# Optimization experiments

Hardware: AMD Instinct MI355X
Metric: run time of the kernel (lower is better)

## Reference

```python
import jax, jax.numpy as jnp
import numpy as np

B, S, E, H = 2, 2048, 1024, 16
DH = E // H  # 64


def setup_inputs() -> dict:
    key = jax.random.key(0)
    ks = jax.random.split(key, 13)
    s = 1.0 / np.sqrt(E)
    inp = {
        'query': jax.random.normal(ks[0], (B, S, E), jnp.float32),
        'key':   jax.random.normal(ks[1], (B, S, E), jnp.float32),
        'value': jax.random.normal(ks[2], (B, S, E), jnp.float32),
        # nn.Linear weights stored [out, in]
        'Wq': jax.random.uniform(ks[3], (E, E), jnp.float32, -s, s),
        'bq': jax.random.uniform(ks[4], (E,), jnp.float32, -s, s),
        'Wk': jax.random.uniform(ks[5], (E, E), jnp.float32, -s, s),
        'bk': jax.random.uniform(ks[6], (E,), jnp.float32, -s, s),
        'Wv': jax.random.uniform(ks[7], (E, E), jnp.float32, -s, s),
        'bv': jax.random.uniform(ks[8], (E,), jnp.float32, -s, s),
        # 1x1 Conv2d over head channels: weight [H, H] (squeezed from [H,H,1,1]), bias [H]
        'Wc': jax.random.uniform(ks[9], (H, H), jnp.float32, -1.0 / np.sqrt(H), 1.0 / np.sqrt(H)),
        'bc': jax.random.uniform(ks[10], (H,), jnp.float32, -1.0 / np.sqrt(H), 1.0 / np.sqrt(H)),
        'Wo': jax.random.uniform(ks[11], (E, E), jnp.float32, -s, s),
        'bo': jax.random.uniform(ks[12], (E,), jnp.float32, -s, s),
    }
    return inp


def reference(query, key, value, Wq, bq, Wk, bk, Wv, bv, Wc, bc, Wo, bo):
    b, s = query.shape[0], query.shape[1]
    # projections -> (B, H, S, Dh)
    def split_heads(x):
        return x.reshape(b, s, H, DH).transpose(0, 2, 1, 3)
    Q = split_heads(query @ Wq.T + bq)
    K = split_heads(key @ Wk.T + bk)
    V = split_heads(value @ Wv.T + bv)
    # raw scores (B, H, S, S)
    scores = jnp.einsum('bhqd,bhkd->bhqk', Q, K) / np.sqrt(DH).astype(np.float32)
    # 1x1 conv mixes logits across heads: channel-wise matmul + bias
    noise = jnp.einsum('gh,bhqk->bgqk', Wc, scores) + bc[None, :, None, None]
    scores = scores + noise
    weights = jax.nn.softmax(scores, axis=-1)
    out = jnp.einsum('bhqk,bhkd->bhqd', weights, V)  # (B, H, S, Dh)
    out = out.transpose(0, 2, 1, 3).reshape(b, s, E)
    return out @ Wo.T + bo
```

## Files before the change

### kernel.cpp

```cpp
#include <hip/hip_runtime.h>


typedef __attribute__((ext_vector_type(8))) short bf16x8_t;
typedef __attribute__((ext_vector_type(4))) float f32x4_t;

__device__ inline unsigned short f2bf(float f) {
  unsigned u = __builtin_bit_cast(unsigned, f);
  u += 0x7fffu + ((u >> 16) & 1u);
  return (unsigned short)(u >> 16);
}

struct ConvArgs {
  const float* src[7];
  unsigned short* dst[7];
  int n[7];
};

__global__ __launch_bounds__(256) void convert_f32_bf16(ConvArgs a) {
  const int which = blockIdx.y;
  const int i = (blockIdx.x * 256 + threadIdx.x) * 8;
  if (i >= a.n[which]) return;
  const float* s = a.src[which] + i;
  f32x4_t x0 = *(const f32x4_t*)(s);
  f32x4_t x1 = *(const f32x4_t*)(s + 4);
  bf16x8_t o;
#pragma unroll
  for (int j = 0; j < 4; j++) o[j] = (short)f2bf(x0[j]);
#pragma unroll
  for (int j = 0; j < 4; j++) o[4 + j] = (short)f2bf(x1[j]);
  *(bf16x8_t*)(a.dst[which] + i) = o;
}

__global__ __launch_bounds__(256) void gemm_bt(
    const unsigned short* __restrict__ A, const unsigned short* __restrict__ Bt,
    const float* __restrict__ bias, void* __restrict__ C,
    int M, int N, int K, int c_is_f32)
{
  __shared__ unsigned short As[128 * 32];
  __shared__ unsigned short Bs[128 * 32];
  const int t = threadIdx.x;
  const int l = t & 63;
  const int w = t >> 6;
  const int quad = l >> 4, n16 = l & 15;
  const int wm = (w & 1) * 64, wn = (w >> 1) * 64;
  const long m0 = (long)blockIdx.x * 128, n0 = (long)blockIdx.y * 128;

  f32x4_t acc[4][4] = {};

  const unsigned short* gA = A + (m0 + (t >> 2)) * (long)K + (t & 3) * 8;
  const unsigned short* gB = Bt + (n0 + (t >> 2)) * (long)K + (t & 3) * 8;
  const long rowskip = 64l * K;

  for (int kt = 0; kt < K; kt += 32) {
    bf16x8_t ra0 = *(const bf16x8_t*)(gA + kt);
    bf16x8_t ra1 = *(const bf16x8_t*)(gA + kt + rowskip);
    bf16x8_t rb0 = *(const bf16x8_t*)(gB + kt);
    bf16x8_t rb1 = *(const bf16x8_t*)(gB + kt + rowskip);
    __syncthreads();
    *(bf16x8_t*)&As[t * 8] = ra0;
    *(bf16x8_t*)&As[2048 + t * 8] = ra1;
    *(bf16x8_t*)&Bs[t * 8] = rb0;
    *(bf16x8_t*)&Bs[2048 + t * 8] = rb1;
    __syncthreads();
    bf16x8_t af[4], bfr[4];
#pragma unroll
    for (int i = 0; i < 4; i++) {
      af[i]  = *(const bf16x8_t*)&As[(wm + i * 16 + n16) * 32 + quad * 8];
      bfr[i] = *(const bf16x8_t*)&Bs[(wn + i * 16 + n16) * 32 + quad * 8];
    }
#pragma unroll
    for (int mi = 0; mi < 4; mi++)
#pragma unroll
      for (int ni = 0; ni < 4; ni++)
        acc[mi][ni] = __builtin_amdgcn_mfma_f32_16x16x32_bf16(af[mi], bfr[ni], acc[mi][ni], 0, 0, 0);
  }

#pragma unroll
  for (int ni = 0; ni < 4; ni++) {
    const long n = n0 + wn + ni * 16 + n16;
    const float bv = bias[n];
#pragma unroll
    for (int mi = 0; mi < 4; mi++) {
#pragma unroll
      for (int r = 0; r < 4; r++) {
        const long m = m0 + wm + mi * 16 + quad * 4 + r;
        const float v = acc[mi][ni][r] + bv;
        if (c_is_f32) ((float*)C)[m * N + n] = v;
        else ((unsigned short*)C)[m * N + n] = f2bf(v);
      }
    }
  }
}

__global__ __launch_bounds__(256) void transpose_v(
    const unsigned short* __restrict__ V, unsigned short* __restrict__ VT)
{
  __shared__ unsigned short tile[64][72];
  const int t = threadIdx.x;
  const int s0 = blockIdx.x * 64, h = blockIdx.y, b = blockIdx.z;
#pragma unroll
  for (int r = 0; r < 2; r++) {
    const int elem = r * 2048 + t * 8;
    const int s = elem >> 6, d = elem & 63;
    *(bf16x8_t*)&tile[s][d] =
        *(const bf16x8_t*)&V[(size_t)(b * 2048 + s0 + s) * 1024 + h * 64 + d];
  }
  __syncthreads();
#pragma unroll
  for (int r = 0; r < 2; r++) {
    const int elem = r * 2048 + t * 8;
    const int d = elem >> 6, sl = elem & 63;
    bf16x8_t o;
#pragma unroll
    for (int j = 0; j < 8; j++) o[j] = (short)tile[sl + j][d];
    *(bf16x8_t*)&VT[((size_t)(b * 16 + h) * 64 + d) * 2048 + s0 + sl] = o;
  }
}

__global__ __launch_bounds__(1024) void attention_fused(
    const unsigned short* __restrict__ Qb, const unsigned short* __restrict__ Kb,
    const unsigned short* __restrict__ VT, const float* __restrict__ Wc,
    unsigned short* __restrict__ Obuf)
{
  __shared__ unsigned short sraw[512 * 40];
  __shared__ float sprime[16 * 580];
  __shared__ unsigned short pbuf[16][16 * 40];
  __shared__ unsigned short mmat[16 * 32];

  const int t = threadIdx.x;
  const int g = t >> 6, l = t & 63;
  const int quad = l >> 4, n16 = l & 15;
  const int qb = blockIdx.x, b = blockIdx.y;
  const int q0 = qb * 16;

  for (int i = t; i < 512 * 40; i += 1024) sraw[i] = 0;
  if (t < 256) {
    const int gg = t >> 4, hh = t & 15;
    const float v = (((gg == hh) ? 1.0f : 0.0f) + Wc[gg * 16 + hh]) * 0.125f;
    mmat[gg * 32 + hh] = f2bf(v);
  } else if (t < 512) {
    const int t2 = t - 256;
    mmat[(t2 >> 4) * 32 + 16 + (t2 & 15)] = 0;
  }
  __syncthreads();

  const bf16x8_t mfrag = *(const bf16x8_t*)&mmat[n16 * 32 + quad * 8];
  bf16x8_t qf[2];
#pragma unroll
  for (int dr = 0; dr < 2; dr++)
    qf[dr] = *(const bf16x8_t*)&Qb[(size_t)(b * 2048 + q0 + n16) * 1024 + g * 64 + dr * 32 + quad * 8];

  f32x4_t o[4] = {};
  float m_run = -1e30f, l_run = 0.0f;
  const int qrow = l >> 2, kpos = (l & 3) * 8;

  for (int kt = 0; kt < 2048; kt += 32) {
    bf16x8_t kf[2][2], vf[4];
#pragma unroll
    for (int kc = 0; kc < 2; kc++)
#pragma unroll
      for (int dr = 0; dr < 2; dr++)
        kf[kc][dr] = *(const bf16x8_t*)&Kb[(size_t)(b * 2048 + kt + kc * 16 + n16) * 1024
                                           + g * 64 + dr * 32 + quad * 8];
#pragma unroll
    for (int dc = 0; dc < 4; dc++)
      vf[dc] = *(const bf16x8_t*)&VT[((size_t)(b * 16 + g) * 64 + dc * 16 + n16) * 2048
                                      + kt + quad * 8];

    f32x4_t sfrag[2] = {};
#pragma unroll
    for (int kc = 0; kc < 2; kc++)
#pragma unroll
      for (int dr = 0; dr < 2; dr++)
        sfrag[kc] = __builtin_amdgcn_mfma_f32_16x16x32_bf16(qf[dr], kf[kc][dr], sfrag[kc], 0, 0, 0);

#pragma unroll
    for (int kc = 0; kc < 2; kc++)
#pragma unroll
      for (int r = 0; r < 4; r++) {
        const int col = (quad * 4 + r) * 32 + kc * 16 + n16;
        sraw[col * 40 + g] = f2bf(sfrag[kc][r]);
      }
    __syncthreads();

    f32x4_t mixd[2];
#pragma unroll
    for (int c2 = 0; c2 < 2; c2++) {
      const int c = g * 2 + c2;
      const bf16x8_t bb = *(const bf16x8_t*)&sraw[(c * 16 + n16) * 40 + quad * 8];
      f32x4_t z = {};
      mixd[c2] = __builtin_amdgcn_mfma_f32_16x16x32_bf16(mfrag, bb, z, 0, 0, 0);
    }
#pragma unroll
    for (int c2 = 0; c2 < 2; c2++) {
      const int c = g * 2 + c2;
      const int qq = c >> 1;
      const int kk = (c & 1) * 16 + n16;
#pragma unroll
      for (int r = 0; r < 4; r++)
        sprime[(quad * 4 + r) * 580 + qq * 36 + kk] = mixd[c2][r];
    }
    __syncthreads();

    const float* rowp = &sprime[g * 580 + qrow * 36 + kpos];
    const f32x4_t x0 = *(const f32x4_t*)rowp;
    const f32x4_t x1 = *(const f32x4_t*)(rowp + 4);
    float mloc = fmaxf(fmaxf(fmaxf(x0[0], x0[1]), fmaxf(x0[2], x0[3])),
                       fmaxf(fmaxf(x1[0], x1[1]), fmaxf(x1[2], x1[3])));
    mloc = fmaxf(mloc, __shfl_xor(mloc, 1));
    mloc = fmaxf(mloc, __shfl_xor(mloc, 2));
    const float mnew = fmaxf(m_run, mloc);
    const float alpha = __expf(m_run - mnew);
    float sum = 0.0f;
    bf16x8_t pv8;
#pragma unroll
    for (int j = 0; j < 4; j++) {
      const float e = __expf(x0[j] - mnew);
      sum += e; pv8[j] = (short)f2bf(e);
    }
#pragma unroll
    for (int j = 0; j < 4; j++) {
      const float e = __expf(x1[j] - mnew);
      sum += e; pv8[4 + j] = (short)f2bf(e);
    }
    sum += __shfl_xor(sum, 1);
    sum += __shfl_xor(sum, 2);
    l_run = l_run * alpha + sum;
    m_run = mnew;
    *(bf16x8_t*)&pbuf[g][qrow * 40 + kpos] = pv8;

#pragma unroll
    for (int r = 0; r < 4; r++) {
      const float ar = __shfl(alpha, (quad * 4 + r) * 4);
#pragma unroll
      for (int dc = 0; dc < 4; dc++) o[dc][r] *= ar;
    }

    const bf16x8_t pf = *(const bf16x8_t*)&pbuf[g][n16 * 40 + quad * 8];
#pragma unroll
    for (int dc = 0; dc < 4; dc++)
      o[dc] = __builtin_amdgcn_mfma_f32_16x16x32_bf16(pf, vf[dc], o[dc], 0, 0, 0);
  }

  float linv[4];
#pragma unroll
  for (int r = 0; r < 4; r++)
    linv[r] = 1.0f / __shfl(l_run, (quad * 4 + r) * 4);
#pragma unroll
  for (int dc = 0; dc < 4; dc++)
#pragma unroll
    for (int r = 0; r < 4; r++) {
      const float v = o[dc][r] * linv[r];
      Obuf[(size_t)(b * 2048 + q0 + quad * 4 + r) * 1024 + g * 64 + dc * 16 + n16] = f2bf(v);
    }
}

extern "C" void kernel_launch(void* const* d_in, const int* in_sizes, int n_in,
                              void* d_out, int out_size, void* d_ws, size_t ws_size,
                              hipStream_t stream) {
  const float* query = (const float*)d_in[0];
  const float* key   = (const float*)d_in[1];
  const float* value = (const float*)d_in[2];
  const float* Wq = (const float*)d_in[3];
  const float* bq = (const float*)d_in[4];
  const float* Wk = (const float*)d_in[5];
  const float* bk = (const float*)d_in[6];
  const float* Wv = (const float*)d_in[7];
  const float* bv = (const float*)d_in[8];
  const float* Wc = (const float*)d_in[9];
  const float* Wo = (const float*)d_in[11];
  const float* bo = (const float*)d_in[12];

  char* ws = (char*)d_ws;
  const size_t MB = 1024 * 1024;
  unsigned short* q_bf  = (unsigned short*)(ws);
  unsigned short* k_bf  = (unsigned short*)(ws + 8 * MB);
  unsigned short* v_bf  = (unsigned short*)(ws + 16 * MB);
  unsigned short* wq_bf = (unsigned short*)(ws + 24 * MB);
  unsigned short* wk_bf = (unsigned short*)(ws + 26 * MB);
  unsigned short* wv_bf = (unsigned short*)(ws + 28 * MB);
  unsigned short* wo_bf = (unsigned short*)(ws + 30 * MB);
  unsigned short* Qb    = (unsigned short*)(ws + 32 * MB);
  unsigned short* Kb    = (unsigned short*)(ws + 40 * MB);
  unsigned short* Vb    = (unsigned short*)(ws + 48 * MB);
  unsigned short* VT   = k_bf;
  unsigned short* Obuf = q_bf;

  ConvArgs ca;
  ca.src[0] = query; ca.dst[0] = q_bf;  ca.n[0] = 2 * 2048 * 1024;
  ca.src[1] = key;   ca.dst[1] = k_bf;  ca.n[1] = 2 * 2048 * 1024;
  ca.src[2] = value; ca.dst[2] = v_bf;  ca.n[2] = 2 * 2048 * 1024;
  ca.src[3] = Wq;    ca.dst[3] = wq_bf; ca.n[3] = 1024 * 1024;
  ca.src[4] = Wk;    ca.dst[4] = wk_bf; ca.n[4] = 1024 * 1024;
  ca.src[5] = Wv;    ca.dst[5] = wv_bf; ca.n[5] = 1024 * 1024;
  ca.src[6] = Wo;    ca.dst[6] = wo_bf; ca.n[6] = 1024 * 1024;
  convert_f32_bf16<<<dim3(2048, 7), 256, 0, stream>>>(ca);

  gemm_bt<<<dim3(32, 8), 256, 0, stream>>>(q_bf, wq_bf, bq, Qb, 4096, 1024, 1024, 0);
  gemm_bt<<<dim3(32, 8), 256, 0, stream>>>(k_bf, wk_bf, bk, Kb, 4096, 1024, 1024, 0);
  gemm_bt<<<dim3(32, 8), 256, 0, stream>>>(v_bf, wv_bf, bv, Vb, 4096, 1024, 1024, 0);

  transpose_v<<<dim3(32, 16, 2), 256, 0, stream>>>(Vb, VT);

  attention_fused<<<dim3(128, 2), 1024, 0, stream>>>(Qb, Kb, VT, Wc, Obuf);

  gemm_bt<<<dim3(32, 8), 256, 0, stream>>>(Obuf, wo_bf, bo, d_out, 4096, 1024, 1024, 1);
}
```

Baseline: 493.7 us.

## Split attention over key halves, fuse activation conversion into GEMMs, use LDS DMA loads

The attention kernel now splits the key dimension into two halves across a third grid axis. Each half writes unnormalised partial outputs plus running max and sum, and a new combine kernel merges them. This doubles the number of blocks from 256 to 512, which should fill the GPU better. The fp32 activations are no longer pre-converted; the projection GEMMs read fp32 A and convert in registers, removing a large conversion pass and its memory traffic. The GEMMs also use global_load_lds for bf16 tiles, and attention replaces the P staging buffer with lane shuffles and shrinks LDS padding. In exchange it adds an extra kernel, extra partial-output traffic, and a bf16 rounding of unnormalised partial outputs.

```diff
diff --git a/kernel.cpp b/kernel.cpp
--- a/kernel.cpp
+++ b/kernel.cpp
@@ -2,24 +2,32 @@
 
 
 typedef __attribute__((ext_vector_type(8))) short bf16x8_t;
+typedef __attribute__((ext_vector_type(4))) short bf16x4_t;
 typedef __attribute__((ext_vector_type(4))) float f32x4_t;
+typedef __attribute__((ext_vector_type(4))) int i32x4_t;
 
 __device__ inline unsigned short f2bf(float f) {
   unsigned u = __builtin_bit_cast(unsigned, f);
   u += 0x7fffu + ((u >> 16) & 1u);
   return (unsigned short)(u >> 16);
 }
+__device__ inline float bf2f(unsigned short u) {
+  unsigned v = ((unsigned)u) << 16;
+  return __builtin_bit_cast(float, v);
+}
+__device__ inline void glds16(const void* g, void* l) {
+  __builtin_amdgcn_global_load_lds((const __attribute__((address_space(1))) void*)g,
+                                   (__attribute__((address_space(3))) void*)l, 16, 0, 0);
+}
 
 struct ConvArgs {
-  const float* src[7];
-  unsigned short* dst[7];
-  int n[7];
+  const float* src[4];
+  unsigned short* dst[4];
 };
 
 __global__ __launch_bounds__(256) void convert_f32_bf16(ConvArgs a) {
   const int which = blockIdx.y;
   const int i = (blockIdx.x * 256 + threadIdx.x) * 8;
-  if (i >= a.n[which]) return;
   const float* s = a.src[which] + i;
   f32x4_t x0 = *(const f32x4_t*)(s);
   f32x4_t x1 = *(const f32x4_t*)(s + 4);
@@ -31,8 +39,9 @@
   *(bf16x8_t*)(a.dst[which] + i) = o;
 }
 
+template <int AF32>
 __global__ __launch_bounds__(256) void gemm_bt(
-    const unsigned short* __restrict__ A, const unsigned short* __restrict__ Bt,
+    const void* __restrict__ Av, const unsigned short* __restrict__ Bt,
     const float* __restrict__ bias, void* __restrict__ C,
     int M, int N, int K, int c_is_f32)
 {
@@ -47,20 +56,36 @@
 
   f32x4_t acc[4][4] = {};
 
-  const unsigned short* gA = A + (m0 + (t >> 2)) * (long)K + (t & 3) * 8;
+  const long rowskip = 64l * (long)K;
   const unsigned short* gB = Bt + (n0 + (t >> 2)) * (long)K + (t & 3) * 8;
-  const long rowskip = 64l * K;
+  const unsigned short* gA16 = nullptr;
+  const float* gA32 = nullptr;
+  if (AF32) gA32 = (const float*)Av + (m0 + (t >> 2)) * (long)K + (t & 3) * 8;
+  else      gA16 = (const unsigned short*)Av + (m0 + (t >> 2)) * (long)K + (t & 3) * 8;
 
   for (int kt = 0; kt < K; kt += 32) {
-    bf16x8_t ra0 = *(const bf16x8_t*)(gA + kt);
-    bf16x8_t ra1 = *(const bf16x8_t*)(gA + kt + rowskip);
-    bf16x8_t rb0 = *(const bf16x8_t*)(gB + kt);
-    bf16x8_t rb1 = *(const bf16x8_t*)(gB + kt + rowskip);
+    f32x4_t a00, a01, a10, a11;
+    if (AF32) {
+      a00 = *(const f32x4_t*)(gA32 + kt);
+      a01 = *(const f32x4_t*)(gA32 + kt + 4);
+      a10 = *(const f32x4_t*)(gA32 + kt + rowskip);
+      a11 = *(const f32x4_t*)(gA32 + kt + rowskip + 4);
+    }
     __syncthreads();
-    *(bf16x8_t*)&As[t * 8] = ra0;
-    *(bf16x8_t*)&As[2048 + t * 8] = ra1;
-    *(bf16x8_t*)&Bs[t * 8] = rb0;
-    *(bf16x8_t*)&Bs[2048 + t * 8] = rb1;
+    glds16(gB + kt, &Bs[w * 512]);
+    glds16(gB + kt + rowskip, &Bs[2048 + w * 512]);
+    if (AF32) {
+      bf16x8_t r0, r1;
+#pragma unroll
+      for (int j = 0; j < 4; j++) { r0[j] = (short)f2bf(a00[j]); r0[4 + j] = (short)f2bf(a01[j]); }
+#pragma unroll
+      for (int j = 0; j < 4; j++) { r1[j] = (short)f2bf(a10[j]); r1[4 + j] = (short)f2bf(a11[j]); }
+      *(bf16x8_t*)&As[t * 8] = r0;
+      *(bf16x8_t*)&As[2048 + t * 8] = r1;
+    } else {
+      glds16(gA16 + kt, &As[w * 512]);
+      glds16(gA16 + kt + rowskip, &As[2048 + w * 512]);
+    }
     __syncthreads();
     bf16x8_t af[4], bfr[4];
 #pragma unroll
@@ -117,27 +142,27 @@
   }
 }
 
-__global__ __launch_bounds__(1024) void attention_fused(
+__global__ __launch_bounds__(1024, 8) void attention_fused(
     const unsigned short* __restrict__ Qb, const unsigned short* __restrict__ Kb,
     const unsigned short* __restrict__ VT, const float* __restrict__ Wc,
-    unsigned short* __restrict__ Obuf)
+    unsigned short* __restrict__ O0, unsigned short* __restrict__ O1,
+    float2* __restrict__ ML)
 {
-  __shared__ unsigned short sraw[512 * 40];
+  __shared__ unsigned short sraw[512 * 36];
   __shared__ float sprime[16 * 580];
-  __shared__ unsigned short pbuf[16][16 * 40];
   __shared__ unsigned short mmat[16 * 32];
 
   const int t = threadIdx.x;
   const int g = t >> 6, l = t & 63;
   const int quad = l >> 4, n16 = l & 15;
-  const int qb = blockIdx.x, b = blockIdx.y;
+  const int qb = blockIdx.x, b = blockIdx.y, khalf = blockIdx.z;
   const int q0 = qb * 16;
-
-  for (int i = t; i < 512 * 40; i += 1024) sraw[i] = 0;
+  const int kt0 = khalf * 1024;
+
+  for (int i = t; i < 512 * 36; i += 1024) sraw[i] = 0;
   if (t < 256) {
     const int gg = t >> 4, hh = t & 15;
-    const float v = (((gg == hh) ? 1.0f : 0.0f) + Wc[gg * 16 + hh]) * 0.125f;
-    mmat[gg * 32 + hh] = f2bf(v);
+    mmat[gg * 32 + hh] = f2bf((((gg == hh) ? 1.0f : 0.0f) + Wc[gg * 16 + hh]) * 0.125f);
   } else if (t < 512) {
     const int t2 = t - 256;
     mmat[(t2 >> 4) * 32 + 16 + (t2 & 15)] = 0;
@@ -154,7 +179,7 @@
   float m_run = -1e30f, l_run = 0.0f;
   const int qrow = l >> 2, kpos = (l & 3) * 8;
 
-  for (int kt = 0; kt < 2048; kt += 32) {
+  for (int kt = kt0; kt < kt0 + 1024; kt += 32) {
     bf16x8_t kf[2][2], vf[4];
 #pragma unroll
     for (int kc = 0; kc < 2; kc++)
@@ -177,29 +202,27 @@
 #pragma unroll
     for (int kc = 0; kc < 2; kc++)
 #pragma unroll
-      for (int r = 0; r < 4; r++) {
-        const int col = (quad * 4 + r) * 32 + kc * 16 + n16;
-        sraw[col * 40 + g] = f2bf(sfrag[kc][r]);
-      }
+      for (int r = 0; r < 4; r++)
+        sraw[((quad * 4 + r) * 32 + kc * 16 + n16) * 36 + g] = f2bf(sfrag[kc][r]);
     __syncthreads();
 
     f32x4_t mixd[2];
 #pragma unroll
     for (int c2 = 0; c2 < 2; c2++) {
-      const int c = g * 2 + c2;
-      const bf16x8_t bb = *(const bf16x8_t*)&sraw[(c * 16 + n16) * 40 + quad * 8];
+      const int rb = ((g * 2 + c2) * 16 + n16) * 36 + quad * 8;
+      const bf16x4_t lo = *(const bf16x4_t*)&sraw[rb];
+      const bf16x4_t hi = *(const bf16x4_t*)&sraw[rb + 4];
+      bf16x8_t bb;
+#pragma unroll
+      for (int j = 0; j < 4; j++) { bb[j] = lo[j]; bb[4 + j] = hi[j]; }
       f32x4_t z = {};
       mixd[c2] = __builtin_amdgcn_mfma_f32_16x16x32_bf16(mfrag, bb, z, 0, 0, 0);
     }
 #pragma unroll
-    for (int c2 = 0; c2 < 2; c2++) {
-      const int c = g * 2 + c2;
-      const int qq = c >> 1;
-      const int kk = (c & 1) * 16 + n16;
+    for (int c2 = 0; c2 < 2; c2++)
 #pragma unroll
       for (int r = 0; r < 4; r++)
-        sprime[(quad * 4 + r) * 580 + qq * 36 + kk] = mixd[c2][r];
-    }
+        sprime[(quad * 4 + r) * 580 + g * 36 + c2 * 16 + n16] = mixd[c2][r];
     __syncthreads();
 
     const float* rowp = &sprime[g * 580 + qrow * 36 + kpos];
@@ -227,7 +250,13 @@
     sum += __shfl_xor(sum, 2);
     l_run = l_run * alpha + sum;
     m_run = mnew;
-    *(bf16x8_t*)&pbuf[g][qrow * 40 + kpos] = pv8;
+
+    const i32x4_t pvi = __builtin_bit_cast(i32x4_t, pv8);
+    const int srcl = n16 * 4 + quad;
+    i32x4_t pfi;
+#pragma unroll
+    for (int j = 0; j < 4; j++) pfi[j] = __shfl(pvi[j], srcl);
+    const bf16x8_t pf = __builtin_bit_cast(bf16x8_t, pfi);
 
 #pragma unroll
     for (int r = 0; r < 4; r++) {
@@ -235,24 +264,45 @@
 #pragma unroll
       for (int dc = 0; dc < 4; dc++) o[dc][r] *= ar;
     }
-
-    const bf16x8_t pf = *(const bf16x8_t*)&pbuf[g][n16 * 40 + quad * 8];
 #pragma unroll
     for (int dc = 0; dc < 4; dc++)
       o[dc] = __builtin_amdgcn_mfma_f32_16x16x32_bf16(pf, vf[dc], o[dc], 0, 0, 0);
   }
 
-  float linv[4];
-#pragma unroll
-  for (int r = 0; r < 4; r++)
-    linv[r] = 1.0f / __shfl(l_run, (quad * 4 + r) * 4);
+  if ((l & 3) == 0) {
+    float2 v; v.x = m_run; v.y = l_run;
+    ML[((size_t)(khalf * 2 + b) * 16 + g) * 2048 + q0 + qrow] = v;
+  }
+  unsigned short* Op = khalf ? O1 : O0;
 #pragma unroll
   for (int dc = 0; dc < 4; dc++)
 #pragma unroll
-    for (int r = 0; r < 4; r++) {
-      const float v = o[dc][r] * linv[r];
-      Obuf[(size_t)(b * 2048 + q0 + quad * 4 + r) * 1024 + g * 64 + dc * 16 + n16] = f2bf(v);
-    }
+    for (int r = 0; r < 4; r++)
+      Op[(size_t)(b * 2048 + q0 + quad * 4 + r) * 1024 + g * 64 + dc * 16 + n16] = f2bf(o[dc][r]);
+}
+
+__global__ __launch_bounds__(256) void combine_halves(
+    const unsigned short* __restrict__ O0, const unsigned short* __restrict__ O1,
+    const float2* __restrict__ ML, unsigned short* __restrict__ Obuf)
+{
+  const int row = blockIdx.x;
+  const int b = row >> 11, q = row & 2047;
+  const int t = threadIdx.x;
+  const int h = t >> 4;
+  const float2 ml0 = ML[((size_t)(b) * 16 + h) * 2048 + q];
+  const float2 ml1 = ML[((size_t)(2 + b) * 16 + h) * 2048 + q];
+  const float M = fmaxf(ml0.x, ml1.x);
+  const float w0 = __expf(ml0.x - M), w1 = __expf(ml1.x - M);
+  const float inv = 1.0f / (w0 * ml0.y + w1 * ml1.y);
+  const size_t base = (size_t)row * 1024 + t * 4;
+  const ushort4 a = *(const ushort4*)&O0[base];
+  const ushort4 c = *(const ushort4*)&O1[base];
+  ushort4 o;
+  o.x = f2bf((w0 * bf2f(a.x) + w1 * bf2f(c.x)) * inv);
+  o.y = f2bf((w0 * bf2f(a.y) + w1 * bf2f(c.y)) * inv);
+  o.z = f2bf((w0 * bf2f(a.z) + w1 * bf2f(c.z)) * inv);
+  o.w = f2bf((w0 * bf2f(a.w) + w1 * bf2f(c.w)) * inv);
+  *(ushort4*)&Obuf[base] = o;
 }
 
 extern "C" void kernel_launch(void* const* d_in, const int* in_sizes, int n_in,
@@ -273,36 +323,35 @@
 
   char* ws = (char*)d_ws;
   const size_t MB = 1024 * 1024;
-  unsigned short* q_bf  = (unsigned short*)(ws);
-  unsigned short* k_bf  = (unsigned short*)(ws + 8 * MB);
-  unsigned short* v_bf  = (unsigned short*)(ws + 16 * MB);
-  unsigned short* wq_bf = (unsigned short*)(ws + 24 * MB);
-  unsigned short* wk_bf = (unsigned short*)(ws + 26 * MB);
-  unsigned short* wv_bf = (unsigned short*)(ws + 28 * MB);
-  unsigned short* wo_bf = (unsigned short*)(ws + 30 * MB);
-  unsigned short* Qb    = (unsigned short*)(ws + 32 * MB);
-  unsigned short* Kb    = (unsigned short*)(ws + 40 * MB);
-  unsigned short* Vb    = (unsigned short*)(ws + 48 * MB);
-  unsigned short* VT   = k_bf;
-  unsigned short* Obuf = q_bf;
+  unsigned short* Qb    = (unsigned short*)(ws);
+  unsigned short* Kb    = (unsigned short*)(ws + 8 * MB);
+  unsigned short* Vb    = (unsigned short*)(ws + 16 * MB);
+  unsigned short* VT    = (unsigned short*)(ws + 24 * MB);
+  unsigned short* Or1   = (unsigned short*)(ws + 32 * MB);
+  float2*         ML    = (float2*)(ws + 40 * MB);
+  unsigned short* wq_bf = (unsigned short*)(ws + 41 * MB);
+  unsigned short* wk_bf = (unsigned short*)(ws + 43 * MB);
+  unsigned short* wv_bf = (unsigned short*)(ws + 45 * MB);
+  unsigned short* wo_bf = (unsigned short*)(ws + 47 * MB);
+  unsigned short* Or0  = Vb;
+  unsigned short* Obuf = Qb;
 
   ConvArgs ca;
-  ca.src[0] = query; ca.dst[0] = q_bf;  ca.n[0] = 2 * 2048 * 1024;
-  ca.src[1] = key;   ca.dst[1] = k_bf;  ca.n[1] = 2 * 2048 * 1024;
-  ca.src[2] = value; ca.dst[2] = v_bf;  ca.n[2] = 2 * 2048 * 1024;
-  ca.src[3] = Wq;    ca.dst[3] = wq_bf; ca.n[3] = 1024 * 1024;
-  ca.src[4] = Wk;    ca.dst[4] = wk_bf; ca.n[4] = 1024 * 1024;
-  ca.src[5] = Wv;    ca.dst[5] = wv_bf; ca.n[5] = 1024 * 1024;
-  ca.src[6] = Wo;    ca.dst[6] = wo_bf; ca.n[6] = 1024 * 1024;
-  convert_f32_bf16<<<dim3(2048, 7), 256, 0, stream>>>(ca);
-
-  gemm_bt<<<dim3(32, 8), 256, 0, stream>>>(q_bf, wq_bf, bq, Qb, 4096, 1024, 1024, 0);
-  gemm_bt<<<dim3(32, 8), 256, 0, stream>>>(k_bf, wk_bf, bk, Kb, 4096, 1024, 1024, 0);
-  gemm_bt<<<dim3(32, 8), 256, 0, stream>>>(v_bf, wv_bf, bv, Vb, 4096, 1024, 1024, 0);
+  ca.src[0] = Wq; ca.dst[0] = wq_bf;
+  ca.src[1] = Wk; ca.dst[1] = wk_bf;
+  ca.src[2] = Wv; ca.dst[2] = wv_bf;
+  ca.src[3] = Wo; ca.dst[3] = wo_bf;
+  convert_f32_bf16<<<dim3(512, 4), 256, 0, stream>>>(ca);
+
+  gemm_bt<1><<<dim3(32, 8), 256, 0, stream>>>(query, wq_bf, bq, Qb, 4096, 1024, 1024, 0);
+  gemm_bt<1><<<dim3(32, 8), 256, 0, stream>>>(key,   wk_bf, bk, Kb, 4096, 1024, 1024, 0);
+  gemm_bt<1><<<dim3(32, 8), 256, 0, stream>>>(value, wv_bf, bv, Vb, 4096, 1024, 1024, 0);
 
   transpose_v<<<dim3(32, 16, 2), 256, 0, stream>>>(Vb, VT);
 
-  attention_fused<<<dim3(128, 2), 1024, 0, stream>>>(Qb, Kb, VT, Wc, Obuf);
-
-  gemm_bt<<<dim3(32, 8), 256, 0, stream>>>(Obuf, wo_bf, bo, d_out, 4096, 1024, 1024, 1);
-}
+  attention_fused<<<dim3(128, 2, 2), 1024, 0, stream>>>(Qb, Kb, VT, Wc, Or0, Or1, ML);
+
+  combine_halves<<<dim3(4096), 256, 0, stream>>>(Or0, Or1, ML, Obuf);
+
+  gemm_bt<0><<<dim3(32, 8), 256, 0, stream>>>(Obuf, wo_bf, bo, d_out, 4096, 1024, 1024, 1);
+}
```

Result: slower. 725.2 us (+46.9%).
